# Kernel optimization log

Measured on AMD Instinct MI355X. Metric: run time of the kernel, lower is better.

Reference implementation:

```python
import jax, jax.numpy as jnp
import numpy as np

B, T, C, H = 4, 1024, 512, 4
D = C // H
N_LAYER, LAYER_ID = 12, 1


def setup_inputs() -> dict:
    key = jax.random.key(0)
    ks = jax.random.split(key, 10)
    w = lambda k, shape: 0.02 * jax.random.normal(k, shape, dtype=jnp.float32)

    r01 = LAYER_ID / (N_LAYER - 1)          # ratio_0_to_1
    r1a0 = 1.0 - LAYER_ID / N_LAYER          # ratio_1_to_almost0
    i = np.arange(C, dtype=np.float32)
    time_decay = (-5.0 + 8.0 * (i / (C - 1)) ** (0.7 + 1.3 * r01)).astype(np.float32)
    xv = i / C
    tm_q = (xv ** r1a0).astype(np.float32)[None, None, :]
    tm_k = (xv ** r1a0).astype(np.float32)[None, None, :]
    tm_v = ((xv ** r1a0) + 0.3 * r01).astype(np.float32)[None, None, :]
    tm_g = (xv ** (0.5 * r1a0)).astype(np.float32)[None, None, :]

    return dict(
        x=jax.random.normal(ks[0], (B, T, C), dtype=jnp.float32),
        ln1_g=jnp.ones((C,), jnp.float32), ln1_b=jnp.zeros((C,), jnp.float32),
        ln2_g=jnp.ones((C,), jnp.float32), ln2_b=jnp.zeros((C,), jnp.float32),
        time_decay=jnp.asarray(time_decay),
        tm_q=jnp.asarray(tm_q), tm_k=jnp.asarray(tm_k),
        tm_v=jnp.asarray(tm_v), tm_g=jnp.asarray(tm_g),
        Wq=w(ks[1], (C, C)), Wk=w(ks[2], (C, C)), Wv=w(ks[3], (C, C)),
        Wg=w(ks[4], (C, C)), Wo=w(ks[5], (C, C)),
        rms_scale=jnp.ones((C,), jnp.float32),
        W1=w(ks[6], (4 * C, C)), W2=w(ks[7], (C, 4 * C)),
    )


def layernorm(x, g, b, eps=1e-5):
    m = x.mean(-1, keepdims=True)
    v = ((x - m) ** 2).mean(-1, keepdims=True)
    return g * (x - m) / jnp.sqrt(v + eps) + b


def rmsnorm(x, scale, eps=1e-8):
    # matches: norm = ||x||_2 / sqrt(dim); out = scale * x / (norm + eps)
    norm = jnp.sqrt(jnp.sum(x * x, axis=-1, keepdims=True)) / (x.shape[-1] ** 0.5)
    return scale * (x / (norm + eps))


def lnssm_scan(q, k, v, lam):
    """Decayed linear-attention scan. q,k,v: [B,T,H,D]; lam: [H,D] (decay over k index).
    Returns S: [B,T,H,D] = q_t^T A_t, Zs: [B,T,H] = q_t . z_t."""
    qT, kT, vT = (jnp.moveaxis(a, 1, 0) for a in (q, k, v))  # [T,B,H,D]
    Bq = q.shape[0]
    A0 = jnp.zeros((Bq, q.shape[2], q.shape[3], q.shape[3]), q.dtype)
    z0 = jnp.zeros((Bq, q.shape[2], q.shape[3]), q.dtype)

    def step(carry, inp):
        A, z = carry
        qt, kt, vt = inp
        A = lam[None, :, :, None] * A + kt[..., None] * vt[..., None, :]  # [B,H,Dk,Dv]
        z = lam[None] * z + kt                                            # [B,H,Dk]
        St = jnp.einsum('bhi,bhij->bhj', qt, A)
        Zt = jnp.einsum('bhi,bhi->bh', qt, z)
        return (A, z), (St, Zt)

    _, (S, Zs) = jax.lax.scan(step, (A0, z0), (qT, kT, vT))
    return jnp.moveaxis(S, 0, 1), jnp.moveaxis(Zs, 0, 1)


def reference(x, ln1_g, ln1_b, ln2_g, ln2_b, time_decay, tm_q, tm_k, tm_v, tm_g,
              Wq, Wk, Wv, Wg, Wo, rms_scale, W1, W2):
    Bx, Tx, Cx = x.shape
    Hh, Dd = H, Cx // H

    # --- TimeMix on ln1(x) ---
    h = layernorm(x, ln1_g, ln1_b)
    xx = jnp.concatenate([jnp.zeros_like(h[:, :1]), h[:, :-1]], axis=1)  # time shift
    xq = h * tm_q + xx * (1 - tm_q)
    xk = h * tm_k + xx * (1 - tm_k)
    xv_ = h * tm_v + xx * (1 - tm_v)
    xg = h * tm_g + xx * (1 - tm_g)
    q = xq @ Wq.T
    k = xk @ Wk.T
    v = xv_ @ Wv.T
    g = jax.nn.sigmoid(xg @ Wg.T)
    q = jnp.exp(rmsnorm(q, rms_scale))
    k = jnp.exp(rmsnorm(k, rms_scale))

    lam = jnp.exp(-jnp.exp(time_decay)).reshape(Hh, Dd)
    qh = q.reshape(Bx, Tx, Hh, Dd)
    kh = k.reshape(Bx, Tx, Hh, Dd)
    vh = v.reshape(Bx, Tx, Hh, Dd)
    S, Zs = lnssm_scan(qh, kh, vh, lam)
    att = (S / Zs[..., None]).reshape(Bx, Tx, Cx)
    att = (g * att) @ Wo.T
    x = x + att

    # --- ChannelMix on ln2(x) ---
    h2 = layernorm(x, ln2_g, ln2_b)
    x = x + jax.nn.gelu(h2 @ W1.T, approximate=False) @ W2.T
    return x
```

## Files before the change

### kernel.cpp

```cpp
#include <hip/hip_runtime.h>
#include <math.h>

#define Bb 4
#define Tt 1024
#define Cc 512
#define Hh 4
#define Dd 128
#define Mrows (Bb*Tt)
#define NC 32
#define CL 32
#define AUGSZ (Dd*(Dd+1))
#define AUGSTRIDE (16*AUGSZ)
#define AUGB_CB 18432

typedef unsigned short u16;
typedef __attribute__((ext_vector_type(8))) short bf16x8;
typedef __attribute__((ext_vector_type(4))) float f32x4;

__device__ __forceinline__ float readlane_f(float v, int lane) {
  return __uint_as_float(__builtin_amdgcn_readlane(__float_as_uint(v), lane));
}
__device__ __forceinline__ u16 f2bf(float f) {
  unsigned u = __float_as_uint(f);
  unsigned r = (u + 0x7fffu + ((u >> 16) & 1u)) >> 16;
  return (u16)r;
}
__device__ __forceinline__ unsigned pack2(float a, float b) {
  return (unsigned)f2bf(a) | ((unsigned)f2bf(b) << 16);
}

__global__ __launch_bounds__(256) void ln_kernel(const float* __restrict__ x,
    const float* __restrict__ g, const float* __restrict__ bta, float* __restrict__ out)
{
  int row = blockIdx.x, tid = threadIdx.x;
  const float* xr = x + (size_t)row * Cc;
  float v0 = xr[tid], v1 = xr[tid + 256];
  float s = v0 + v1, s2 = v0*v0 + v1*v1;
  #pragma unroll
  for (int off = 32; off > 0; off >>= 1) {
    s  += __shfl_down(s,  off, 64);
    s2 += __shfl_down(s2, off, 64);
  }
  __shared__ float rs[4], rq[4];
  int w = tid >> 6;
  if ((tid & 63) == 0) { rs[w] = s; rq[w] = s2; }
  __syncthreads();
  float S  = rs[0]+rs[1]+rs[2]+rs[3];
  float S2 = rq[0]+rq[1]+rq[2]+rq[3];
  float mean = S * (1.0f/Cc);
  float var  = S2 * (1.0f/Cc) - mean*mean;
  float inv = rsqrtf(var + 1e-5f);
  out[(size_t)row*Cc + tid]       = g[tid]     * (v0-mean)*inv + bta[tid];
  out[(size_t)row*Cc + tid + 256] = g[tid+256] * (v1-mean)*inv + bta[tid+256];
}

__global__ __launch_bounds__(256) void ln2b_kernel(const float* __restrict__ x,
    const float* __restrict__ p0, const float* __restrict__ p1,
    const float* __restrict__ g, const float* __restrict__ bta,
    float* __restrict__ x1, u16* __restrict__ out)
{
  int row = blockIdx.x, tid = threadIdx.x;
  size_t r0 = (size_t)row * Cc + tid, r1 = r0 + 256;
  float v0 = x[r0] + p0[r0] + p1[r0];
  float v1 = x[r1] + p0[r1] + p1[r1];
  x1[r0] = v0; x1[r1] = v1;
  float s = v0 + v1, s2 = v0*v0 + v1*v1;
  #pragma unroll
  for (int off = 32; off > 0; off >>= 1) {
    s  += __shfl_down(s,  off, 64);
    s2 += __shfl_down(s2, off, 64);
  }
  __shared__ float rs[4], rq[4];
  int w = tid >> 6;
  if ((tid & 63) == 0) { rs[w] = s; rq[w] = s2; }
  __syncthreads();
  float S  = rs[0]+rs[1]+rs[2]+rs[3];
  float S2 = rq[0]+rq[1]+rq[2]+rq[3];
  float mean = S * (1.0f/Cc);
  float var  = S2 * (1.0f/Cc) - mean*mean;
  float inv = rsqrtf(var + 1e-5f);
  int c0 = tid, c1 = tid + 256;
  float o0 = g[c0] * (v0-mean)*inv + bta[c0];
  float o1 = g[c1] * (v1-mean)*inv + bta[c1];
  out[((size_t)(c0 >> 3) * Mrows + row) * 8 + (c0 & 7)] = f2bf(o0);
  out[((size_t)(c1 >> 3) * Mrows + row) * 8 + (c1 & 7)] = f2bf(o1);
}

__device__ __forceinline__ void mix_one(const float* tm, int c0,
    float4 ha, float4 hb, float4 xa, float4 xb, u16* dst, size_t i8)
{
  float4 ta = *(const float4*)(tm + c0);
  float4 tb = *(const float4*)(tm + c0 + 4);
  uint4 o;
  o.x = pack2(ha.x*ta.x + xa.x*(1.f-ta.x), ha.y*ta.y + xa.y*(1.f-ta.y));
  o.y = pack2(ha.z*ta.z + xa.z*(1.f-ta.z), ha.w*ta.w + xa.w*(1.f-ta.w));
  o.z = pack2(hb.x*tb.x + xb.x*(1.f-tb.x), hb.y*tb.y + xb.y*(1.f-tb.y));
  o.w = pack2(hb.z*tb.z + xb.z*(1.f-tb.z), hb.w*tb.w + xb.w*(1.f-tb.w));
  *(uint4*)(dst + i8) = o;
}

__global__ __launch_bounds__(256) void mix_kernel(const float* __restrict__ h,
    const float* __restrict__ tmq, const float* __restrict__ tmk,
    const float* __restrict__ tmv, const float* __restrict__ tmg,
    u16* __restrict__ xqb, u16* __restrict__ xkb,
    u16* __restrict__ xvb, u16* __restrict__ xgb)
{
  int i = blockIdx.x * 256 + threadIdx.x;
  int m = i & 4095, c0 = (i >> 12) << 3;
  const float* hp = h + (size_t)m*Cc + c0;
  float4 ha = *(const float4*)hp, hb = *(const float4*)(hp + 4);
  float4 xa = make_float4(0,0,0,0), xb = make_float4(0,0,0,0);
  if (m & 1023) { xa = *(const float4*)(hp - Cc); xb = *(const float4*)(hp - Cc + 4); }
  size_t i8 = (size_t)i * 8;
  mix_one(tmq, c0, ha, hb, xa, xb, xqb, i8);
  mix_one(tmk, c0, ha, hb, xa, xb, xkb, i8);
  mix_one(tmv, c0, ha, hb, xa, xb, xvb, i8);
  mix_one(tmg, c0, ha, hb, xa, xb, xgb, i8);
}

__global__ __launch_bounds__(256) void wconv_kernel(const float* __restrict__ src,
    u16* __restrict__ out, int K, int nshift)
{
  int i = blockIdx.x * 256 + threadIdx.x;
  int n = i & ((1 << nshift) - 1), kg = i >> nshift;
  const float* p = src + (size_t)n * K + kg * 8;
  float4 a = *(const float4*)p, b = *(const float4*)(p + 4);
  uint4 o;
  o.x = pack2(a.x, a.y); o.y = pack2(a.z, a.w);
  o.z = pack2(b.x, b.y); o.w = pack2(b.z, b.w);
  *(uint4*)(out + (size_t)i * 8) = o;
}

__global__ __launch_bounds__(256) void wconv5_kernel(const float* __restrict__ s0,
    const float* __restrict__ s1, const float* __restrict__ s2,
    const float* __restrict__ s3, const float* __restrict__ s4,
    u16* __restrict__ out)
{
  int wsel = blockIdx.x >> 7;
  const float* src = wsel == 0 ? s0 : wsel == 1 ? s1 : wsel == 2 ? s2 : wsel == 3 ? s3 : s4;
  int i = (blockIdx.x & 127) * 256 + threadIdx.x;
  int n = i & 511, kg = i >> 9;
  const float* p = src + (size_t)n * 512 + kg * 8;
  float4 a = *(const float4*)p, b = *(const float4*)(p + 4);
  uint4 o;
  o.x = pack2(a.x, a.y); o.y = pack2(a.z, a.w);
  o.z = pack2(b.x, b.y); o.w = pack2(b.z, b.w);
  *(uint4*)(out + (size_t)wsel * 262144 + (size_t)i * 8) = o;
}

template<int MR, int NR, int KR>
__device__ __forceinline__ void gemm_core(const u16* __restrict__ A,
    const u16* __restrict__ W, const float* __restrict__ res,
    float* __restrict__ outf, u16* __restrict__ outb, int act,
    int m0, int n0, u16* Asm, u16* Bsm)
{
  const int tid = threadIdx.x, w = tid >> 6, l = tid & 63;
  const int wr = w >> 1, wc = w & 1;
  f32x4 acc[4][4];
  #pragma unroll
  for (int i = 0; i < 4; ++i)
    #pragma unroll
    for (int j = 0; j < 4; ++j) acc[i][j] = (f32x4){0.f,0.f,0.f,0.f};
  const int kgl = l >> 4, rl = l & 15;
  const int q = w * 4;

  #define STAGE(KT, BUF) do {                                               \
    _Pragma("unroll")                                                       \
    for (int ii = 0; ii < 4; ++ii) {                                        \
      int qq = q + ii;                                                      \
      int isB = qq >> 3, idx = qq & 7, kg = idx >> 1, hf = idx & 1;         \
      const u16* src = isB                                                  \
        ? W + ((size_t)((KT)*4 + kg) * NR + n0 + hf*64 + l) * 8             \
        : A + ((size_t)((KT)*4 + kg) * MR + m0 + hf*64 + l) * 8;            \
      u16* dst = (isB ? Bsm : Asm) + (BUF)*4096 + (kg * 128 + hf * 64) * 8; \
      __builtin_amdgcn_global_load_lds(                                     \
          (const __attribute__((address_space(1))) void*)src,               \
          (__attribute__((address_space(3))) void*)dst, 16, 0, 0);          \
    }                                                                       \
  } while (0)

  constexpr int nk = KR >> 5;
  STAGE(0, 0); STAGE(1, 1); STAGE(2, 2);
  for (int kt = 0; kt < nk; ++kt) {
    const int cur = kt & 3;
    if (kt < nk - 2)       asm volatile("s_waitcnt vmcnt(8)" ::: "memory");
    else if (kt == nk - 2) asm volatile("s_waitcnt vmcnt(4)" ::: "memory");
    else                   asm volatile("s_waitcnt vmcnt(0)" ::: "memory");
    __builtin_amdgcn_s_barrier();
    bf16x8 af[4], bfr[4];
    #pragma unroll
    for (int f = 0; f < 4; ++f)
      af[f] = *(const bf16x8*)&Asm[cur*4096 + (kgl*128 + wr*64 + f*16 + rl) * 8];
    #pragma unroll
    for (int f = 0; f < 4; ++f)
      bfr[f] = *(const bf16x8*)&Bsm[cur*4096 + (kgl*128 + wc*64 + f*16 + rl) * 8];
    if (kt + 3 < nk) STAGE(kt + 3, (kt + 3) & 3);
    __builtin_amdgcn_s_setprio(1);
    #pragma unroll
    for (int i = 0; i < 4; ++i)
      #pragma unroll
      for (int j = 0; j < 4; ++j)
        acc[i][j] = __builtin_amdgcn_mfma_f32_16x16x32_bf16(af[i], bfr[j], acc[i][j], 0, 0, 0);
    __builtin_amdgcn_s_setprio(0);
  }
  #undef STAGE

  const int rbase = (l >> 4) * 4, cn = l & 15;
  #pragma unroll
  for (int i = 0; i < 4; ++i) {
    #pragma unroll
    for (int j = 0; j < 4; ++j) {
      #pragma unroll
      for (int r = 0; r < 4; ++r) {
        int m = m0 + wr*64 + i*16 + rbase + r;
        int n = n0 + wc*64 + j*16 + cn;
        float vv = acc[i][j][r];
        if (res) vv += res[(size_t)m * NR + n];
        if (act == 1) vv = 0.5f*vv*(1.f + erff(vv * 0.70710678118f));
        else if (act == 2) vv = 1.f/(1.f + expf(-vv));
        if (outb) outb[((size_t)(n >> 3) * MR + m) * 8 + (n & 7)] = f2bf(vv);
        else outf[(size_t)m * NR + n] = vv;
      }
    }
  }
}

__global__ __launch_bounds__(256) void gemm_qkvg(const u16* __restrict__ xall,
    const u16* __restrict__ Wall, float* __restrict__ outall)
{
  __shared__ __align__(16) u16 Asm[4*4096];
  __shared__ __align__(16) u16 Bsm[4*4096];
  int z = blockIdx.z;
  const size_t E = (size_t)Mrows * Cc;
  gemm_core<Mrows,512,512>(xall + z*E, Wall + (size_t)z*262144, nullptr,
            outall + z*E, nullptr, z == 3 ? 2 : 0,
            blockIdx.y * 128, blockIdx.x * 128, Asm, Bsm);
}

__global__ __launch_bounds__(256) void gemm_wo(const u16* __restrict__ A,
    const u16* __restrict__ W, float* __restrict__ pbuf)
{
  __shared__ __align__(16) u16 Asm[4*4096];
  __shared__ __align__(16) u16 Bsm[4*4096];
  int z = blockIdx.z;
  const size_t E = (size_t)Mrows * Cc;
  gemm_core<Mrows,512,256>(A + (size_t)z*32*Mrows*8, W + (size_t)z*32*512*8, nullptr,
            pbuf + z*E, nullptr, 0, blockIdx.y * 128, blockIdx.x * 128, Asm, Bsm);
}

__global__ __launch_bounds__(256) void gemm_w1(const u16* __restrict__ A,
    const u16* __restrict__ W, u16* __restrict__ outb)
{
  __shared__ __align__(16) u16 Asm[4*4096];
  __shared__ __align__(16) u16 Bsm[4*4096];
  gemm_core<Mrows,2048,512>(A, W, nullptr, nullptr, outb, 1,
            blockIdx.y * 128, blockIdx.x * 128, Asm, Bsm);
}

__global__ __launch_bounds__(256) void gemm_w2(const u16* __restrict__ A,
    const u16* __restrict__ W, float* __restrict__ pbuf)
{
  __shared__ __align__(16) u16 Asm[4*4096];
  __shared__ __align__(16) u16 Bsm[4*4096];
  int z = blockIdx.z;
  const size_t E = (size_t)Mrows * Cc;
  gemm_core<Mrows,512,512>(A + (size_t)z*64*Mrows*8, W + (size_t)z*64*512*8, nullptr,
            pbuf + z*E, nullptr, 0, blockIdx.y * 128, blockIdx.x * 128, Asm, Bsm);
}

__global__ __launch_bounds__(256) void reduce4_kernel(const float* __restrict__ x1,
    const float* __restrict__ p, float* __restrict__ out)
{
  const size_t E = (size_t)Mrows * Cc;
  size_t f = ((size_t)blockIdx.x * 256 + threadIdx.x) * 4;
  float4 a = *(const float4*)(x1 + f);
  float4 q0 = *(const float4*)(p + f);
  float4 q1 = *(const float4*)(p + E + f);
  float4 q2 = *(const float4*)(p + 2*E + f);
  float4 q3 = *(const float4*)(p + 3*E + f);
  float4 o;
  o.x = a.x + q0.x + q1.x + q2.x + q3.x;
  o.y = a.y + q0.y + q1.y + q2.y + q3.y;
  o.z = a.z + q0.z + q1.z + q2.z + q3.z;
  o.w = a.w + q0.w + q1.w + q2.w + q3.w;
  *(float4*)(out + f) = o;
}

__global__ __launch_bounds__(256) void rmsexp_kernel(float* __restrict__ qm,
    float* __restrict__ km, const float* __restrict__ scale)
{
  int row = blockIdx.x, tid = threadIdx.x;
  float* xr = (blockIdx.y ? km : qm) + (size_t)row * Cc;
  float v0 = xr[tid], v1 = xr[tid+256];
  float s2 = v0*v0 + v1*v1;
  #pragma unroll
  for (int off = 32; off > 0; off >>= 1) s2 += __shfl_down(s2, off, 64);
  __shared__ float rq[4];
  int w = tid >> 6;
  if ((tid & 63) == 0) rq[w] = s2;
  __syncthreads();
  float S2 = rq[0]+rq[1]+rq[2]+rq[3];
  float norm = sqrtf(S2) * 0.044194173824159216f;
  float r = 1.f / (norm + 1e-8f);
  xr[tid]     = expf(scale[tid]     * v0 * r);
  xr[tid+256] = expf(scale[tid+256] * v1 * r);
}

__global__ __launch_bounds__(256) void chunk_state_kernel(const float* __restrict__ k,
    const float* __restrict__ v, const float* __restrict__ td, float* __restrict__ Aug)
{
  __shared__ float k_lds[CL][Dd];
  __shared__ float v_lds[CL][Dd];
  int blk = blockIdx.x; int c = blk & (NC-1); int bh = blk >> 5;
  int b = bh >> 2, h = bh & 3;
  int tid = threadIdx.x;
  size_t base = ((size_t)b*Tt + (size_t)c*CL)*Cc + h*Dd;
  #pragma unroll
  for (int r = 0; r < 4; ++r) {
    int idx4 = r*256 + tid;
    int s = idx4 >> 5; int i4 = (idx4 & 31) << 2;
    *(float4*)&k_lds[s][i4] = *(const float4*)&k[base + (size_t)s*Cc + i4];
    *(float4*)&v_lds[s][i4] = *(const float4*)&v[base + (size_t)s*Cc + i4];
  }
  __syncthreads();
  int iq = tid >> 3; int i0 = iq << 2;
  int jg = tid & 7;  int j0 = jg << 4;
  float lam4[4], powv[4], zacc[4];
  #pragma unroll
  for (int ci=0; ci<4; ++ci) {
    lam4[ci] = expf(-expf(td[h*Dd + i0 + ci]));
    powv[ci] = 1.f; zacc[ci] = 0.f;
  }
  float acc[4][16];
  #pragma unroll
  for (int ci=0; ci<4; ++ci)
    #pragma unroll
    for (int jj=0; jj<16; ++jj) acc[ci][jj] = 0.f;

  for (int s = CL-1; s >= 0; --s) {
    float4 k4 = *(const float4*)&k_lds[s][i0];
    float kw0 = powv[0]*k4.x, kw1 = powv[1]*k4.y, kw2 = powv[2]*k4.z, kw3 = powv[3]*k4.w;
    zacc[0]+=kw0; zacc[1]+=kw1; zacc[2]+=kw2; zacc[3]+=kw3;
    #pragma unroll
    for (int q4 = 0; q4 < 4; ++q4) {
      float4 v4 = *(const float4*)&v_lds[s][j0 + q4*4];
      float vv[4] = {v4.x, v4.y, v4.z, v4.w};
      #pragma unroll
      for (int u=0; u<4; ++u) {
        acc[0][q4*4+u] += kw0*vv[u];
        acc[1][q4*4+u] += kw1*vv[u];
        acc[2][q4*4+u] += kw2*vv[u];
        acc[3][q4*4+u] += kw3*vv[u];
      }
    }
    powv[0]*=lam4[0]; powv[1]*=lam4[1]; powv[2]*=lam4[2]; powv[3]*=lam4[3];
  }
  float* aug = Aug + ((size_t)c*16 + bh)*AUGSZ;
  #pragma unroll
  for (int jj=0; jj<16; ++jj) {
    int j = j0 + jj;
    float4 wv = make_float4(acc[0][jj], acc[1][jj], acc[2][jj], acc[3][jj]);
    *(float4*)&aug[(size_t)j*Dd + i0] = wv;
  }
  if (jg == 0)
    *(float4*)&aug[(size_t)Dd*Dd + i0] = make_float4(zacc[0],zacc[1],zacc[2],zacc[3]);
}

__global__ __launch_bounds__(256) void combine_kernel(const float* __restrict__ Aug,
    const float* __restrict__ td, u16* __restrict__ Augb)
{
  int idx = blockIdx.x*256 + threadIdx.x;
  int bh = blockIdx.y; int h = bh & 3;
  int j = idx >> 7, i = idx & 127;
  size_t aoff = (size_t)(i >> 3) * 1152 + (size_t)j * 8 + (i & 7);
  if (j >= 129) {
    for (int c = 0; c < NC; ++c)
      Augb[((size_t)c*16 + bh)*AUGB_CB + aoff] = 0;
    return;
  }
  float lamL = expf(-expf(td[h*Dd + i]) * (float)CL);
  const float* p = Aug + (size_t)bh*AUGSZ + (size_t)j*Dd + i;
  float prev = 0.f;
  for (int c = 0; c < NC; ++c) {
    float val = p[(size_t)c*AUGSTRIDE];
    Augb[((size_t)c*16 + bh)*AUGB_CB + aoff] = f2bf(prev);
    prev = lamL*prev + val;
  }
}

__global__ __launch_bounds__(256, 2) void scan_mfma_kernel(
    const float* __restrict__ q, const float* __restrict__ k,
    const float* __restrict__ v, const float* __restrict__ td,
    const u16* __restrict__ Augb, const float* __restrict__ gmat,
    u16* __restrict__ out)
{
  __shared__ float k_lds[32*192];
  __shared__ u16  qfrag[32*128];
  __shared__ u16  vfrag[4*1152];
  __shared__ float P32[32*33];
  __shared__ u16  pfrag[32*32];
  __shared__ float lam_lds[128];
  __shared__ float zbuf[32];

  const int tid = threadIdx.x;
  const int blk = blockIdx.x; const int c = blk & 31, bh = blk >> 5;
  const int b = bh >> 2, h = bh & 3;
  const int w = tid >> 6, l = tid & 63;
  const int t = (w << 3) + (l >> 3);
  const int is = l & 7;

  if (tid < 128) lam_lds[tid] = expf(-expf(td[h*Dd + tid]));

  const size_t rowbase = ((size_t)(b*Tt + c*CL + t))*Cc + h*Dd + is*16;

  float qv[16];
  {
    #pragma unroll
    for (int c4 = 0; c4 < 4; ++c4) {
      float4 q4 = *(const float4*)(q + rowbase + c4*4);
      qv[c4*4+0]=q4.x; qv[c4*4+1]=q4.y; qv[c4*4+2]=q4.z; qv[c4*4+3]=q4.w;
    }
    float lt = (float)(t + 1);
    u16 qt[16];
    #pragma unroll
    for (int e = 0; e < 16; ++e) {
      float el2 = -expf(td[h*Dd + is*16 + e]) * 1.4426950408889634f;
      qt[e] = f2bf(qv[e] * exp2f(el2 * lt));
    }
    #pragma unroll
    for (int hf = 0; hf < 2; ++hf) {
      int k8 = is*2 + hf;
      uint4 pk;
      pk.x = (unsigned)qt[hf*8+0] | ((unsigned)qt[hf*8+1]<<16);
      pk.y = (unsigned)qt[hf*8+2] | ((unsigned)qt[hf*8+3]<<16);
      pk.z = (unsigned)qt[hf*8+4] | ((unsigned)qt[hf*8+5]<<16);
      pk.w = (unsigned)qt[hf*8+6] | ((unsigned)qt[hf*8+7]<<16);
      *(uint4*)&qfrag[t*128 + ((k8 ^ (t&7))<<3)] = pk;
    }
  }
  #pragma unroll
  for (int c4 = 0; c4 < 4; ++c4)
    *(float4*)&k_lds[t*192 + is*24 + c4*4] = *(const float4*)(k + rowbase + c4*4);
  #pragma unroll
  for (int c4 = 0; c4 < 4; ++c4) {
    float4 v4 = *(const float4*)(v + rowbase + c4*4);
    int j0 = is*16 + c4*4;
    vfrag[(t>>3)*1152 + (j0+0)*8 + (t&7)] = f2bf(v4.x);
    vfrag[(t>>3)*1152 + (j0+1)*8 + (t&7)] = f2bf(v4.y);
    vfrag[(t>>3)*1152 + (j0+2)*8 + (t&7)] = f2bf(v4.z);
    vfrag[(t>>3)*1152 + (j0+3)*8 + (t&7)] = f2bf(v4.w);
  }
  if (tid < 32) vfrag[(tid>>3)*1152 + 128*8 + (tid&7)] = 0x3F80;
  if (tid < 240) {
    #pragma unroll
    for (int u = 0; u < 2; ++u) {
      int e = tid*2 + u;
      int ig = e / 120, rem = e % 120;
      vfrag[ig*1152 + (129 + rem/8)*8 + (rem&7)] = 0;
    }
  }
  __syncthreads();

  {
    float lamr[16], wrun[16];
    #pragma unroll
    for (int e4 = 0; e4 < 4; ++e4) {
      float4 l4 = *(const float4*)&lam_lds[is*16 + e4*4];
      lamr[e4*4+0]=l4.x; lamr[e4*4+1]=l4.y; lamr[e4*4+2]=l4.z; lamr[e4*4+3]=l4.w;
    }
    #pragma unroll
    for (int e = 0; e < 16; ++e) wrun[e] = 1.f;
    const int smax = (w << 3) + 7;
    for (int s = smax; s >= 0; --s) {
      float dot = 0.f;
      #pragma unroll
      for (int c4 = 0; c4 < 4; ++c4) {
        float4 k4 = *(const float4*)&k_lds[s*192 + is*24 + c4*4];
        dot = fmaf(qv[c4*4+0], k4.x*wrun[c4*4+0], dot);
        dot = fmaf(qv[c4*4+1], k4.y*wrun[c4*4+1], dot);
        dot = fmaf(qv[c4*4+2], k4.z*wrun[c4*4+2], dot);
        dot = fmaf(qv[c4*4+3], k4.w*wrun[c4*4+3], dot);
      }
      dot += __shfl_xor(dot, 1);
      dot += __shfl_xor(dot, 2);
      dot += __shfl_xor(dot, 4);
      bool act = (s <= t);
      if (act && is == 0) P32[t*33 + s] = dot;
      if (act) {
        #pragma unroll
        for (int e = 0; e < 16; ++e) wrun[e] *= lamr[e];
      }
    }
  }
  __syncthreads();
  {
    int tt = tid >> 3, s0 = (tid & 7) * 4;
    #pragma unroll
    for (int ss = 0; ss < 4; ++ss) {
      int s = s0 + ss;
      float val = (s <= tt) ? P32[tt*33 + s] : 0.f;
      pfrag[tt*32 + (((s>>3) ^ (tt&3))<<3) + (s&7)] = f2bf(val);
    }
  }
  __syncthreads();

  const int tau = w >> 1;
  const int jt0 = (w & 1) ? 5 : 0;
  const int njt = (w & 1) ? 4 : 5;
  const int rl = l & 15, kg = l >> 4;
  const int trow = tau*16 + rl;
  const u16* augb_base = Augb + ((size_t)c*16 + bh)*AUGB_CB;

  bf16x8 aq[4];
  #pragma unroll
  for (int kk = 0; kk < 4; ++kk)
    aq[kk] = *(const bf16x8*)&qfrag[trow*128 + ((((kk<<2)+kg) ^ (trow&7))<<3)];
  bf16x8 ap = *(const bf16x8*)&pfrag[trow*32 + ((kg ^ (trow&3))<<3)];

  f32x4 acc[5];
  #pragma unroll
  for (int u = 0; u < 5; ++u) acc[u] = (f32x4){0.f,0.f,0.f,0.f};

  #pragma unroll
  for (int u = 0; u < 5; ++u) {
    if (u < njt) {
      int jt = jt0 + u;
      #pragma unroll
      for (int kk = 0; kk < 4; ++kk) {
        bf16x8 bfr = *(const bf16x8*)&augb_base[(size_t)(((kk<<2)+kg)*1152 + (jt*16 + rl)*8)];
        acc[u] = __builtin_amdgcn_mfma_f32_16x16x32_bf16(aq[kk], bfr, acc[u], 0, 0, 0);
      }
      bf16x8 bv = *(const bf16x8*)&vfrag[kg*1152 + (jt*16 + rl)*8];
      acc[u] = __builtin_amdgcn_mfma_f32_16x16x32_bf16(ap, bv, acc[u], 0, 0, 0);
    }
  }
  if ((w & 1) && rl == 0) {
    #pragma unroll
    for (int r = 0; r < 4; ++r) zbuf[tau*16 + kg*4 + r] = acc[3][r];
  }
  __syncthreads();

  const int nout = (w & 1) ? 3 : 5;
  #pragma unroll
  for (int u = 0; u < 5; ++u) {
    if (u < nout) {
      int jt = jt0 + u;
      int cc = h*Dd + jt*16 + rl;
      #pragma unroll
      for (int r = 0; r < 4; ++r) {
        int tr = tau*16 + kg*4 + r;
        int m = b*Tt + c*CL + tr;
        float zv = zbuf[tr];
        float gv = gmat[(size_t)m*Cc + cc];
        out[((size_t)(cc >> 3) * Mrows + m) * 8 + (cc & 7)] = f2bf(gv * acc[u][r] / zv);
      }
    }
  }
}

extern "C" void kernel_launch(void* const* d_in, const int* in_sizes, int n_in,
                              void* d_out, int out_size, void* d_ws, size_t ws_size,
                              hipStream_t stream) {
  const float* x    = (const float*)d_in[0];
  const float* ln1g = (const float*)d_in[1];
  const float* ln1b = (const float*)d_in[2];
  const float* ln2g = (const float*)d_in[3];
  const float* ln2b = (const float*)d_in[4];
  const float* td   = (const float*)d_in[5];
  const float* tmq  = (const float*)d_in[6];
  const float* tmk  = (const float*)d_in[7];
  const float* tmv  = (const float*)d_in[8];
  const float* tmg  = (const float*)d_in[9];
  const float* Wq   = (const float*)d_in[10];
  const float* Wk   = (const float*)d_in[11];
  const float* Wv   = (const float*)d_in[12];
  const float* Wg   = (const float*)d_in[13];
  const float* Wo   = (const float*)d_in[14];
  const float* rsc  = (const float*)d_in[15];
  const float* W1   = (const float*)d_in[16];
  const float* W2   = (const float*)d_in[17];
  float* ws = (float*)d_ws;
  const size_t E = (size_t)Mrows*Cc;
  float* s0 = ws;
  float* s1 = ws + E;
  float* s2 = ws + 2*E;
  float* s3 = ws + 3*E;
  float* x1 = ws + 4*E;
  u16* xqb = (u16*)(ws + 5*E);
  u16* xkb = xqb + E;
  u16* xvb = xkb + E;
  u16* xgb = xvb + E;
  float* Aug = ws + 7*E;
  u16* midb = (u16*)Aug;
  float* wreg = ws + 7*E + (size_t)NC*16*AUGSZ;
  u16* Wqb = (u16*)wreg;
  u16* W1b = Wqb + 5*262144;
  u16* W2b = W1b + 1048576;
  u16* Wob = Wqb + 4*262144;
  u16* Augb = W2b + 1048576;
  u16* gattb = xqb;
  u16* h2b   = xkb;

  wconv5_kernel<<<640,256,0,stream>>>(Wq, Wk, Wv, Wg, Wo, Wqb);
  wconv_kernel<<<512,256,0,stream>>>(W1, W1b, 512, 11);
  wconv_kernel<<<512,256,0,stream>>>(W2, W2b, 2048, 9);

  ln_kernel<<<Mrows,256,0,stream>>>(x, ln1g, ln1b, s0);
  mix_kernel<<<1024,256,0,stream>>>(s0, tmq,tmk,tmv,tmg, xqb,xkb,xvb,xgb);
  gemm_qkvg<<<dim3(4,32,4),256,0,stream>>>(xqb, Wqb, s0);
  rmsexp_kernel<<<dim3(Mrows,2),256,0,stream>>>(s0, s1, rsc);
  chunk_state_kernel<<<16*NC,256,0,stream>>>(s1, s2, td, Aug);
  combine_kernel<<<dim3(72,16),256,0,stream>>>(Aug, td, Augb);
  scan_mfma_kernel<<<16*NC,256,0,stream>>>(s0, s1, s2, td, Augb, s3, gattb);
  gemm_wo<<<dim3(4,32,2),256,0,stream>>>(gattb, Wob, s2);
  ln2b_kernel<<<Mrows,256,0,stream>>>(x, s2, s3, ln2g, ln2b, x1, h2b);
  gemm_w1<<<dim3(16,32),256,0,stream>>>(h2b, W1b, midb);
  gemm_w2<<<dim3(4,32,4),256,0,stream>>>(midb, W2b, s0);
  reduce4_kernel<<<2048,256,0,stream>>>(x1, s0, (float*)d_out);
}
```

Baseline: 173.8 us.

## Merge weight conversion launches and shrink GEMM pipeline to three LDS stages

```diff
diff --git a/kernel.cpp b/kernel.cpp
--- a/kernel.cpp
+++ b/kernel.cpp
@@ -118,34 +118,31 @@
   mix_one(tmg, c0, ha, hb, xa, xb, xgb, i8);
 }
 
-__global__ __launch_bounds__(256) void wconv_kernel(const float* __restrict__ src,
-    u16* __restrict__ out, int K, int nshift)
-{
-  int i = blockIdx.x * 256 + threadIdx.x;
+__global__ __launch_bounds__(256) void wconv_all_kernel(
+    const float* __restrict__ Wq, const float* __restrict__ Wk,
+    const float* __restrict__ Wv, const float* __restrict__ Wg,
+    const float* __restrict__ Wo, const float* __restrict__ W1,
+    const float* __restrict__ W2, u16* __restrict__ out)
+{
+  int blk = blockIdx.x;
+  const float* src; u16* dst; int K, nshift;
+  if (blk < 640) {
+    int wsel = blk >> 7;
+    src = wsel==0?Wq:wsel==1?Wk:wsel==2?Wv:wsel==3?Wg:Wo;
+    dst = out + (size_t)wsel*262144; K = 512; nshift = 9; blk &= 127;
+  } else if (blk < 1152) {
+    src = W1; dst = out + (size_t)5*262144; K = 512; nshift = 11; blk -= 640;
+  } else {
+    src = W2; dst = out + (size_t)5*262144 + 1048576; K = 2048; nshift = 9; blk -= 1152;
+  }
+  int i = blk*256 + threadIdx.x;
   int n = i & ((1 << nshift) - 1), kg = i >> nshift;
   const float* p = src + (size_t)n * K + kg * 8;
   float4 a = *(const float4*)p, b = *(const float4*)(p + 4);
   uint4 o;
   o.x = pack2(a.x, a.y); o.y = pack2(a.z, a.w);
   o.z = pack2(b.x, b.y); o.w = pack2(b.z, b.w);
-  *(uint4*)(out + (size_t)i * 8) = o;
-}
-
-__global__ __launch_bounds__(256) void wconv5_kernel(const float* __restrict__ s0,
-    const float* __restrict__ s1, const float* __restrict__ s2,
-    const float* __restrict__ s3, const float* __restrict__ s4,
-    u16* __restrict__ out)
-{
-  int wsel = blockIdx.x >> 7;
-  const float* src = wsel == 0 ? s0 : wsel == 1 ? s1 : wsel == 2 ? s2 : wsel == 3 ? s3 : s4;
-  int i = (blockIdx.x & 127) * 256 + threadIdx.x;
-  int n = i & 511, kg = i >> 9;
-  const float* p = src + (size_t)n * 512 + kg * 8;
-  float4 a = *(const float4*)p, b = *(const float4*)(p + 4);
-  uint4 o;
-  o.x = pack2(a.x, a.y); o.y = pack2(a.z, a.w);
-  o.z = pack2(b.x, b.y); o.w = pack2(b.z, b.w);
-  *(uint4*)(out + (size_t)wsel * 262144 + (size_t)i * 8) = o;
+  *(uint4*)(dst + (size_t)i * 8) = o;
 }
 
 template<int MR, int NR, int KR>
@@ -180,12 +177,11 @@
   } while (0)
 
   constexpr int nk = KR >> 5;
-  STAGE(0, 0); STAGE(1, 1); STAGE(2, 2);
+  STAGE(0, 0); STAGE(1, 1);
+  int cur = 0;
   for (int kt = 0; kt < nk; ++kt) {
-    const int cur = kt & 3;
-    if (kt < nk - 2)       asm volatile("s_waitcnt vmcnt(8)" ::: "memory");
-    else if (kt == nk - 2) asm volatile("s_waitcnt vmcnt(4)" ::: "memory");
-    else                   asm volatile("s_waitcnt vmcnt(0)" ::: "memory");
+    if (kt == nk - 1) asm volatile("s_waitcnt vmcnt(0)" ::: "memory");
+    else              asm volatile("s_waitcnt vmcnt(4)" ::: "memory");
     __builtin_amdgcn_s_barrier();
     bf16x8 af[4], bfr[4];
     #pragma unroll
@@ -194,7 +190,10 @@
     #pragma unroll
     for (int f = 0; f < 4; ++f)
       bfr[f] = *(const bf16x8*)&Bsm[cur*4096 + (kgl*128 + wc*64 + f*16 + rl) * 8];
-    if (kt + 3 < nk) STAGE(kt + 3, (kt + 3) & 3);
+    if (kt + 2 < nk) {
+      int nb = cur + 2; if (nb >= 3) nb -= 3;
+      STAGE(kt + 2, nb);
+    }
     __builtin_amdgcn_s_setprio(1);
     #pragma unroll
     for (int i = 0; i < 4; ++i)
@@ -202,6 +201,7 @@
       for (int j = 0; j < 4; ++j)
         acc[i][j] = __builtin_amdgcn_mfma_f32_16x16x32_bf16(af[i], bfr[j], acc[i][j], 0, 0, 0);
     __builtin_amdgcn_s_setprio(0);
+    if (++cur == 3) cur = 0;
   }
   #undef STAGE
 
@@ -228,8 +228,8 @@
 __global__ __launch_bounds__(256) void gemm_qkvg(const u16* __restrict__ xall,
     const u16* __restrict__ Wall, float* __restrict__ outall)
 {
-  __shared__ __align__(16) u16 Asm[4*4096];
-  __shared__ __align__(16) u16 Bsm[4*4096];
+  __shared__ __align__(16) u16 Asm[3*4096];
+  __shared__ __align__(16) u16 Bsm[3*4096];
   int z = blockIdx.z;
   const size_t E = (size_t)Mrows * Cc;
   gemm_core<Mrows,512,512>(xall + z*E, Wall + (size_t)z*262144, nullptr,
@@ -240,8 +240,8 @@
 __global__ __launch_bounds__(256) void gemm_wo(const u16* __restrict__ A,
     const u16* __restrict__ W, float* __restrict__ pbuf)
 {
-  __shared__ __align__(16) u16 Asm[4*4096];
-  __shared__ __align__(16) u16 Bsm[4*4096];
+  __shared__ __align__(16) u16 Asm[3*4096];
+  __shared__ __align__(16) u16 Bsm[3*4096];
   int z = blockIdx.z;
   const size_t E = (size_t)Mrows * Cc;
   gemm_core<Mrows,512,256>(A + (size_t)z*32*Mrows*8, W + (size_t)z*32*512*8, nullptr,
@@ -251,8 +251,8 @@
 __global__ __launch_bounds__(256) void gemm_w1(const u16* __restrict__ A,
     const u16* __restrict__ W, u16* __restrict__ outb)
 {
-  __shared__ __align__(16) u16 Asm[4*4096];
-  __shared__ __align__(16) u16 Bsm[4*4096];
+  __shared__ __align__(16) u16 Asm[3*4096];
+  __shared__ __align__(16) u16 Bsm[3*4096];
   gemm_core<Mrows,2048,512>(A, W, nullptr, nullptr, outb, 1,
             blockIdx.y * 128, blockIdx.x * 128, Asm, Bsm);
 }
@@ -260,8 +260,8 @@
 __global__ __launch_bounds__(256) void gemm_w2(const u16* __restrict__ A,
     const u16* __restrict__ W, float* __restrict__ pbuf)
 {
-  __shared__ __align__(16) u16 Asm[4*4096];
-  __shared__ __align__(16) u16 Bsm[4*4096];
+  __shared__ __align__(16) u16 Asm[3*4096];
+  __shared__ __align__(16) u16 Bsm[3*4096];
   int z = blockIdx.z;
   const size_t E = (size_t)Mrows * Cc;
   gemm_core<Mrows,512,512>(A + (size_t)z*64*Mrows*8, W + (size_t)z*64*512*8, nullptr,
@@ -601,9 +601,7 @@
   u16* gattb = xqb;
   u16* h2b   = xkb;
 
-  wconv5_kernel<<<640,256,0,stream>>>(Wq, Wk, Wv, Wg, Wo, Wqb);
-  wconv_kernel<<<512,256,0,stream>>>(W1, W1b, 512, 11);
-  wconv_kernel<<<512,256,0,stream>>>(W2, W2b, 2048, 9);
+  wconv_all_kernel<<<1664,256,0,stream>>>(Wq, Wk, Wv, Wg, Wo, W1, W2, Wqb);
 
   ln_kernel<<<Mrows,256,0,stream>>>(x, ln1g, ln1b, s0);
   mix_kernel<<<1024,256,0,stream>>>(s0, tmq,tmk,tmv,tmg, xqb,xkb,xvb,xgb);
```

Result: faster. 168.3 us (-3.2%).
